# Kernel optimization log

Hardware: AMD Instinct MI355X
Metric: run time of the kernel (lower is better)

The kernel has to match this reference:

```python
import jax, jax.numpy as jnp
import numpy as np
from jax import lax

B, N, S, K, C, OUT = 8, 4096, 1024, 24, 64, 128
IN = 2 * C + 3  # 131: grouped(C+3) concat anchor feature(C)
EPS_BN = 1e-5


def _bn_params(key, c):
    k1, k2, k3, k4 = jax.random.split(key, 4)
    gamma = jax.random.uniform(k1, (c,), minval=0.5, maxval=1.5)
    beta = jax.random.normal(k2, (c,)) * 0.1
    mean = jax.random.normal(k3, (c,)) * 0.1
    var = jax.random.uniform(k4, (c,), minval=0.5, maxval=1.5)
    return jnp.stack([gamma, beta, mean, var])  # [4,c]


def setup_inputs() -> dict:
    key = jax.random.key(0)
    ks = jax.random.split(key, 20)
    w = lambda k, shp: jax.random.normal(k, shp) * 0.05
    inp = {
        "xyz": jax.random.normal(ks[0], (B, N, 3)),
        "points": jax.random.normal(ks[1], (B, N, C)),
        "affine_alpha": jnp.ones((1, 1, 1, C + 3)),
        "affine_beta": jnp.zeros((1, 1, 1, C + 3)),
        "transfer_w": w(ks[2], (OUT, IN)),
        "transfer_b": jnp.zeros((OUT,)),
        "transfer_bn": _bn_params(ks[3], OUT),
        "pre_w1": w(ks[4], (2, OUT, OUT)),
        "pre_b1": jnp.zeros((2, OUT)),
        "pre_bn1": jnp.stack([_bn_params(ks[5], OUT), _bn_params(ks[6], OUT)]),
        "pre_w2": w(ks[7], (2, OUT, OUT)),
        "pre_b2": jnp.zeros((2, OUT)),
        "pre_bn2": jnp.stack([_bn_params(ks[8], OUT), _bn_params(ks[9], OUT)]),
        "pos_w1": w(ks[10], (2, OUT, OUT)),
        "pos_b1": jnp.zeros((2, OUT)),
        "pos_bn1": jnp.stack([_bn_params(ks[11], OUT), _bn_params(ks[12], OUT)]),
        "pos_w2": w(ks[13], (2, OUT, OUT)),
        "pos_b2": jnp.zeros((2, OUT)),
        "pos_bn2": jnp.stack([_bn_params(ks[14], OUT), _bn_params(ks[15], OUT)]),
    }
    return inp


def _gather(x, idx):
    # x: [B,N,D], idx: [B,...] -> [B,...,D]
    return jax.vmap(lambda a, i: a[i])(x, idx)


def _sqdist(a, b):
    # a: [B,S,3], b: [B,N,3] -> [B,S,N]
    return (jnp.sum(a * a, -1)[:, :, None] + jnp.sum(b * b, -1)[:, None, :]
            - 2.0 * jnp.einsum('bsd,bnd->bsn', a, b))


def _fps(xyz, s):
    # furthest point sampling, starts at index 0 (matches CUDA pointnet2 impl)
    b, n, _ = xyz.shape
    def step(carry, _):
        dist, last = carry
        p = jnp.take_along_axis(xyz, last[:, None, None], axis=1)  # [B,1,3]
        d = jnp.sum((xyz - p) ** 2, -1)
        dist = jnp.minimum(dist, d)
        nxt = jnp.argmax(dist, axis=-1).astype(jnp.int32)
        return (dist, nxt), nxt
    init = (jnp.full((b, n), 1e10, xyz.dtype), jnp.zeros((b,), jnp.int32))
    _, idxs = lax.scan(step, init, None, length=s - 1)  # [S-1,B]
    return jnp.concatenate([jnp.zeros((1, b), jnp.int32), idxs], 0).T  # [B,S]


def _conv_bn(x, w, b, bn, act=True):
    # 1x1 Conv1d + BatchNorm (eval mode) + optional ReLU. x: [M,Cin,L]
    y = jnp.einsum('oc,mcl->mol', w, x) + b[None, :, None]
    g, be, mu, var = bn[0], bn[1], bn[2], bn[3]
    y = (y - mu[None, :, None]) * (g[None, :, None] / jnp.sqrt(var[None, :, None] + EPS_BN)) + be[None, :, None]
    return jax.nn.relu(y) if act else y


def _res_block(x, w1, b1, bn1, w2, b2, bn2):
    y = _conv_bn(x, w1, b1, bn1, act=True)
    y = _conv_bn(y, w2, b2, bn2, act=False)
    return jax.nn.relu(y + x)


def reference(xyz, points, affine_alpha, affine_beta,
              transfer_w, transfer_b, transfer_bn,
              pre_w1, pre_b1, pre_bn1, pre_w2, pre_b2, pre_bn2,
              pos_w1, pos_b1, pos_bn1, pos_w2, pos_b2, pos_bn2):
    b, n, _ = xyz.shape
    # ---- LocalGrouper ----
    fps_idx = _fps(xyz, S)                      # [B,S]
    new_xyz = _gather(xyz, fps_idx)             # [B,S,3]
    new_points = _gather(points, fps_idx)       # [B,S,C]
    d = _sqdist(new_xyz, xyz)                   # [B,S,N]
    _, idx = lax.top_k(-d, K)                   # k nearest -> [B,S,K]
    grouped_xyz = _gather(xyz, idx)             # [B,S,K,3]
    grouped_points = _gather(points, idx)       # [B,S,K,C]
    grouped = jnp.concatenate([grouped_points, grouped_xyz], -1)  # [B,S,K,C+3]
    # anchor normalize
    mean = jnp.concatenate([new_points, new_xyz], -1)[:, :, None, :]
    diff = grouped - mean
    std = jnp.std(diff.reshape(b, -1), axis=-1, ddof=1)[:, None, None, None]
    grouped = affine_alpha * (diff / (std + 1e-5)) + affine_beta
    anchor = jnp.broadcast_to(new_points[:, :, None, :], (b, S, K, C))
    feats = jnp.concatenate([grouped, anchor], -1)  # [B,S,K,2C+3]
    # ---- PreExtraction ----
    x = feats.transpose(0, 1, 3, 2).reshape(b * S, IN, K)  # [B*S,131,K]
    x = _conv_bn(x, transfer_w, transfer_b, transfer_bn, act=True)
    for i in range(2):
        x = _res_block(x, pre_w1[i], pre_b1[i], pre_bn1[i], pre_w2[i], pre_b2[i], pre_bn2[i])
    x = jnp.max(x, axis=-1)                     # adaptive max pool over K
    x = x.reshape(b, S, OUT).transpose(0, 2, 1)  # [B,OUT,S]
    # ---- PosExtraction ----
    for i in range(2):
        x = _res_block(x, pos_w1[i], pos_b1[i], pos_bn1[i], pos_w2[i], pos_b2[i], pos_bn2[i])
    return x  # [B,128,1024]
```

## Files before the change

### kernel.cpp

```cpp
#include <hip/hip_runtime.h>
#include <hip/hip_bf16.h>
#include <stdint.h>
#include <math.h>

#define DEVINL static __device__ __forceinline__

static constexpr int BB = 8, NN = 4096, SS = 1024, KK = 24, CC = 64;
static constexpr int INCH = 131, OUTCH = 128;

typedef __attribute__((ext_vector_type(8))) short short8v;
typedef __attribute__((ext_vector_type(4))) float f32x4;

#define MFMA16(a, b, c) __builtin_amdgcn_mfma_f32_16x16x32_bf16(a, b, c, 0, 0, 0)

DEVINL unsigned short f2bf(float v) {
  __hip_bfloat16 h = __float2bfloat16(v);
  return *reinterpret_cast<unsigned short*>(&h);
}
DEVINL float bfbits2f(unsigned short u) {
  unsigned x = ((unsigned)u) << 16;
  return __int_as_float(x);
}

__global__ __launch_bounds__(256) void k_prep_xyz(
    const float* __restrict__ xyz,
    float* __restrict__ xs, float* __restrict__ ys,
    float* __restrict__ zs, float* __restrict__ sb) {
  int e = blockIdx.x * 256 + threadIdx.x;
  if (e >= BB * NN) return;
  float x = xyz[e * 3 + 0];
  float y = xyz[e * 3 + 1];
  float z = xyz[e * 3 + 2];
  xs[e] = x; ys[e] = y; zs[e] = z;
  sb[e] = __fadd_rn(__fadd_rn(__fmul_rn(x, x), __fmul_rn(y, y)), __fmul_rn(z, z));
}

__global__ __launch_bounds__(256) void k_prep_w(
    const float* __restrict__ tw,
    const float* __restrict__ pw1, const float* __restrict__ pw2,
    const float* __restrict__ qw1, const float* __restrict__ qw2,
    const float* __restrict__ tb,  const float* __restrict__ tbn,
    const float* __restrict__ pb1, const float* __restrict__ pbn1,
    const float* __restrict__ pb2, const float* __restrict__ pbn2,
    const float* __restrict__ qb1, const float* __restrict__ qbn1,
    const float* __restrict__ qb2, const float* __restrict__ qbn2,
    float* __restrict__ wt_sq, float* __restrict__ bnsb,
    unsigned short* __restrict__ wfhi, unsigned short* __restrict__ wflo) {
  int e = blockIdx.x * 256 + threadIdx.x;
  const int NSQ = 8 * 128 * 128;
  const int NBN = 9 * 128;
  const int NFR = 168 * 64;
  if (e < NSQ) {
    int layer = e >> 14, m = e & 16383;
    int ci = m >> 7, co = m & 127;
    const float* src;
    switch (layer) {
      case 0: src = pw1;         break;
      case 1: src = pw2;         break;
      case 2: src = pw1 + 16384; break;
      case 3: src = pw2 + 16384; break;
      case 4: src = qw1;         break;
      case 5: src = qw2;         break;
      case 6: src = qw1 + 16384; break;
      default: src = qw2 + 16384; break;
    }
    wt_sq[layer * 16384 + ci * 128 + co] = src[co * 128 + ci];
  } else if (e < NSQ + NBN) {
    int r = e - NSQ;
    int L = r >> 7, co = r & 127;
    const float *bn, *bc;
    switch (L) {
      case 0: bn = tbn;        bc = tb;        break;
      case 1: bn = pbn1;       bc = pb1;       break;
      case 2: bn = pbn2;       bc = pb2;       break;
      case 3: bn = pbn1 + 512; bc = pb1 + 128; break;
      case 4: bn = pbn2 + 512; bc = pb2 + 128; break;
      case 5: bn = qbn1;       bc = qb1;       break;
      case 6: bn = qbn2;       bc = qb2;       break;
      case 7: bn = qbn1 + 512; bc = qb1 + 128; break;
      default: bn = qbn2 + 512; bc = qb2 + 128; break;
    }
    float g  = bn[co];
    float be = bn[128 + co];
    float mu = bn[256 + co];
    float va = bn[384 + co];
    float bcv = bc[co];
    float sc = g / sqrtf(va + 1e-5f);
    float bi = (bcv - mu) * sc + be;
    bnsb[L * 256 + co] = sc;
    bnsb[L * 256 + 128 + co] = bi;
  } else if (e < NSQ + NBN + NFR) {
    int r = e - (NSQ + NBN);
    int T = r >> 6, lane = r & 63;
    int L, ks, mt;
    if (T < 40) { L = 0; ks = T >> 3; mt = T & 7; }
    else { int r2 = T - 40; L = 1 + (r2 >> 5); int r3 = r2 & 31; ks = r3 >> 3; mt = r3 & 7; }
    const float* src;
    int K, stride;
    switch (L) {
      case 0:  src = tw;          K = 131; stride = 131; break;
      case 1:  src = pw1;         K = 128; stride = 128; break;
      case 2:  src = pw2;         K = 128; stride = 128; break;
      case 3:  src = pw1 + 16384; K = 128; stride = 128; break;
      default: src = pw2 + 16384; K = 128; stride = 128; break;
    }
    int m = lane & 15, kb = lane >> 4;
    int co = mt * 16 + m;
    int base = (T * 64 + lane) * 8;
#pragma unroll
    for (int j = 0; j < 8; j++) {
      int ci = ks * 32 + kb * 8 + j;
      float w = (ci < K) ? src[co * stride + ci] : 0.f;
      unsigned short h = f2bf(w);
      unsigned short l = f2bf(w - bfbits2f(h));
      wfhi[base + j] = h;
      wflo[base + j] = l;
    }
  }
}

DEVINL float wave_max_f32_l63(float x) {
#define STEPF(C)                                                                \
  {                                                                             \
    int o = __builtin_amdgcn_update_dpp(0xff800000, __float_as_int(x), C, 0xf, 0xf, false); \
    x = fmaxf(x, __int_as_float(o));                                            \
  }
  STEPF(0x111) STEPF(0x112) STEPF(0x114) STEPF(0x118) STEPF(0x142) STEPF(0x143)
#undef STEPF
  return x;
}

__global__ __launch_bounds__(256, 1) void k_fps(
    const float* __restrict__ xs, const float* __restrict__ ys,
    const float* __restrict__ zs, const float* __restrict__ sb,
    const float* __restrict__ points,
    float* __restrict__ nxyz, float* __restrict__ sa, float* __restrict__ newp) {
  __shared__ float lxl[NN], lyl[NN], lzl[NN];
  __shared__ unsigned long long pk[2][4];
  __shared__ int fpsl[SS];
  const int b = blockIdx.x, t = threadIdx.x;
  const int wid = t >> 6, lane = t & 63;
  const float* bx = xs + b * NN;
  const float* by = ys + b * NN;
  const float* bz = zs + b * NN;
  float rx[16], ry[16], rz[16], d[16];
  const int n0 = t * 16;
#pragma unroll
  for (int j = 0; j < 16; j++) {
    rx[j] = bx[n0 + j]; ry[j] = by[n0 + j]; rz[j] = bz[n0 + j];
    lxl[n0 + j] = rx[j]; lyl[n0 + j] = ry[j]; lzl[n0 + j] = rz[j];
    d[j] = 1e10f;
  }
  __syncthreads();
  float px = lxl[0], py = lyl[0], pz = lzl[0];
  if (t == 0) fpsl[0] = 0;
#pragma unroll 1
  for (int i = 1; i < SS; i++) {
    float bestval = -1.f;
    int bestn = 0;
#pragma unroll
    for (int j = 0; j < 16; j++) {
      float dx = __fsub_rn(rx[j], px);
      float dy = __fsub_rn(ry[j], py);
      float dz = __fsub_rn(rz[j], pz);
      float dd = __fadd_rn(__fadd_rn(__fmul_rn(dx, dx), __fmul_rn(dy, dy)),
                           __fmul_rn(dz, dz));
      float nd = fminf(d[j], dd);
      d[j] = nd;
      if (nd > bestval) { bestval = nd; bestn = n0 + j; }
    }
    float wmax = __int_as_float(
        __builtin_amdgcn_readlane(__float_as_int(wave_max_f32_l63(bestval)), 63));
    unsigned long long el = __ballot(bestval == wmax);
    int fl = (int)__ffsll(el) - 1;
    int wn = __builtin_amdgcn_readlane(bestn, fl);
    if (lane == 0)
      pk[i & 1][wid] = ((unsigned long long)__float_as_uint(wmax) << 32) |
                       (unsigned)(NN - 1 - wn);
    __syncthreads();
    const unsigned long long* P = pk[i & 1];
    unsigned long long k0 = P[0], k1 = P[1], k2 = P[2], k3 = P[3];
    unsigned long long m01 = k1 > k0 ? k1 : k0;
    unsigned long long m23 = k3 > k2 ? k3 : k2;
    unsigned long long g = m23 > m01 ? m23 : m01;
    int n = NN - 1 - (int)(unsigned)g;
    px = lxl[n]; py = lyl[n]; pz = lzl[n];
    if (t == 0) fpsl[i] = n;
  }
  __syncthreads();
  for (int s = t; s < SS; s += 256) {
    int row = fpsl[s];
    nxyz[(b * SS + s) * 3 + 0] = lxl[row];
    nxyz[(b * SS + s) * 3 + 1] = lyl[row];
    nxyz[(b * SS + s) * 3 + 2] = lzl[row];
    sa[b * SS + s] = sb[b * NN + row];
  }
  for (int e = t; e < SS * CC; e += 256) {
    int s = e >> 6, c = e & 63;
    int row = fpsl[s];
    newp[(b * SS + s) * CC + c] = points[(b * NN + row) * CC + c];
  }
}

__global__ __launch_bounds__(256, 2) void k_knn(
    const float* __restrict__ xs, const float* __restrict__ ys,
    const float* __restrict__ zs,
    const float* __restrict__ nxyz, const float* __restrict__ sa,
    const float* __restrict__ points, const float* __restrict__ newp,
    int* __restrict__ knn, double* __restrict__ spart) {
  __shared__ float lx[NN], ly[NN], lz[NN];
  __shared__ int selk[4][KK];
  const int blk = blockIdx.x, t = threadIdx.x, wid = t >> 6, lane = t & 63;
  const int b = blk >> 8;
  for (int e = t; e < NN; e += 256) {
    lx[e] = xs[b * NN + e]; ly[e] = ys[b * NN + e]; lz[e] = zs[b * NN + e];
  }
  __syncthreads();
  const int q = blk * 4 + wid;
  float qx = nxyz[q * 3 + 0], qy = nxyz[q * 3 + 1], qz = nxyz[q * 3 + 2];
  float qa = sa[q];
  unsigned keys[64];
#pragma unroll
  for (int j = 0; j < 64; j++) {
    int n = j * 64 + lane;
    float x = lx[n], y = ly[n], z = lz[n];
    float sbn = __fadd_rn(__fadd_rn(__fmul_rn(x, x), __fmul_rn(y, y)), __fmul_rn(z, z));
    float dot = __fadd_rn(__fadd_rn(__fmul_rn(qx, x), __fmul_rn(qy, y)), __fmul_rn(qz, z));
    float dd = __fsub_rn(__fadd_rn(qa, sbn), __fmul_rn(2.0f, dot));
    unsigned u = __float_as_uint(dd);
    u ^= (0x80000000u | (unsigned)((int)u >> 31));
    keys[j] = u;
  }
#pragma unroll 1
  for (int r = 0; r < KK; r++) {
    unsigned bv = keys[0];
    int bj = 0;
#pragma unroll
    for (int j = 1; j < 64; j++) {
      if (keys[j] < bv) { bv = keys[j]; bj = j; }
    }
    unsigned long long gk = ((unsigned long long)bv << 32) | (unsigned)(bj * 64 + lane);
#pragma unroll
    for (int m = 1; m < 64; m <<= 1) {
      unsigned long long o = __shfl_xor(gk, m);
      gk = o < gk ? o : gk;
    }
    int n = (int)(unsigned)gk;
    if (lane == 0) { knn[q * KK + r] = n; selk[wid][r] = n; }
    if (lane == (n & 63)) {
      int jj = n >> 6;
#pragma unroll
      for (int j = 0; j < 64; j++)
        if (j == jj) keys[j] = 0xFFFFFFFFu;
    }
  }
  double s1 = 0.0, s2 = 0.0;
#pragma unroll 1
  for (int i = 0; i < 26; i++) {
    int e = lane + 64 * i;
    if (e < KK * 67) {
      int k = e / 67, c = e - k * 67;
      int n = selk[wid][k];
      float g, mm;
      if (c < CC) {
        g = points[(b * NN + n) * CC + c];
        mm = newp[q * CC + c];
      } else {
        int cc = c - CC;
        g = cc == 0 ? lx[n] : (cc == 1 ? ly[n] : lz[n]);
        mm = nxyz[q * 3 + cc];
      }
      float v = __fsub_rn(g, mm);
      s1 += (double)v;
      s2 += (double)v * (double)v;
    }
  }
#pragma unroll
  for (int m = 1; m < 64; m <<= 1) {
    s1 += __shfl_xor(s1, m);
    s2 += __shfl_xor(s2, m);
  }
  if (lane == 0) { spart[q * 2 + 0] = s1; spart[q * 2 + 1] = s2; }
}

__global__ __launch_bounds__(256) void k_stdfin(
    const double* __restrict__ spart, float* __restrict__ stdp) {
  __shared__ double a1[256], a2[256];
  const int b = blockIdx.x, t = threadIdx.x;
  double s1 = 0.0, s2 = 0.0;
  for (int i = t; i < SS; i += 256) {
    s1 += spart[(b * SS + i) * 2 + 0];
    s2 += spart[(b * SS + i) * 2 + 1];
  }
  a1[t] = s1; a2[t] = s2;
  __syncthreads();
  for (int w = 128; w > 0; w >>= 1) {
    if (t < w) { a1[t] += a1[t + w]; a2[t] += a2[t + w]; }
    __syncthreads();
  }
  if (t == 0) {
    const double n = (double)SS * KK * 67;
    double m = a1[0] / n;
    double var = (a2[0] - a1[0] * m) / (n - 1.0);
    if (var < 0.0) var = 0.0;
    float stdf = (float)sqrt(var);
    stdp[b] = stdf + 1e-5f;
  }
}

static constexpr int BST = 168;
static constexpr int XST = 132;

__global__ __launch_bounds__(256, 3) void k_pre(
    const float* __restrict__ points,
    const float* __restrict__ alpha, const float* __restrict__ beta,
    const float* __restrict__ xs, const float* __restrict__ ys, const float* __restrict__ zs,
    const float* __restrict__ nxyz, const float* __restrict__ newp,
    const float* __restrict__ stdp, const int* __restrict__ knn,
    const unsigned short* __restrict__ wfhi, const unsigned short* __restrict__ wflo,
    const float* __restrict__ bnsb, float* __restrict__ pre_out) {
  __shared__ unsigned short Bhi[32 * BST];
  __shared__ unsigned short Blo[32 * BST];
  __shared__ float Xres[32 * XST];
  __shared__ int kn[KK];
  __shared__ float npl[CC], nxl[3], al[67], bt[67];
  __shared__ float stds;
  const int q = blockIdx.x, b = q >> 10, t = threadIdx.x;
  for (int e = t; e < 32 * BST; e += 256) { Bhi[e] = 0; Blo[e] = 0; }
  if (t < KK) kn[t] = knn[q * KK + t];
  if (t < 67) { al[t] = alpha[t]; bt[t] = beta[t]; }
  if (t < CC) npl[t] = newp[q * CC + t];
  if (t < 3) nxl[t] = nxyz[q * 3 + t];
  if (t == 0) stds = stdp[b];
  __syncthreads();
  for (int e = t; e < KK * 67; e += 256) {
    int k = e / 67, c = e - k * 67;
    int n = kn[k];
    float g, mm;
    if (c < CC) {
      g = points[(b * NN + n) * CC + c];
      mm = npl[c];
    } else {
      int cc = c - CC;
      g = cc == 0 ? xs[b * NN + n] : (cc == 1 ? ys[b * NN + n] : zs[b * NN + n]);
      mm = nxl[cc];
    }
    float v = __fsub_rn(g, mm);
    float tt = __fdiv_rn(v, stds);
    float val = __fadd_rn(__fmul_rn(al[c], tt), bt[c]);
    unsigned short h = f2bf(val);
    Bhi[k * BST + c] = h;
    Blo[k * BST + c] = f2bf(val - bfbits2f(h));
  }
  for (int e = t; e < CC * KK; e += 256) {
    int c = e / KK, k = e - c * KK;
    float val = npl[c];
    unsigned short h = f2bf(val);
    Bhi[k * BST + 67 + c] = h;
    Blo[k * BST + 67 + c] = f2bf(val - bfbits2f(h));
  }
  __syncthreads();

  const int wv = t >> 6, lane = t & 63;
  const int g4 = lane >> 4;
  const int l15 = lane & 15;
  const int mt0 = wv * 2;

#pragma unroll 1
  for (int L = 0; L < 5; ++L) {
    const int nks = (L == 0) ? 5 : 4;
    const int wtb = (L == 0) ? 0 : (8 + 32 * L);
    const bool addres = (L == 2) || (L == 4);
    const bool wres = (L == 0) || (L == 2);
    const bool pool = (L == 4);
    f32x4 acc00 = {0.f, 0.f, 0.f, 0.f}, acc01 = {0.f, 0.f, 0.f, 0.f};
    f32x4 acc10 = {0.f, 0.f, 0.f, 0.f}, acc11 = {0.f, 0.f, 0.f, 0.f};
#pragma unroll 1
    for (int ks = 0; ks < nks; ++ks) {
      const int tb = (wtb + ks * 8 + mt0) * 64 + lane;
      short8v wh0 = *(const short8v*)(wfhi + tb * 8);
      short8v wh1 = *(const short8v*)(wfhi + (tb + 64) * 8);
      short8v wl0 = *(const short8v*)(wflo + tb * 8);
      short8v wl1 = *(const short8v*)(wflo + (tb + 64) * 8);
      const int bo = l15 * BST + ks * 32 + g4 * 8;
      short8v bh0 = *(const short8v*)&Bhi[bo];
      short8v bh1 = *(const short8v*)&Bhi[bo + 16 * BST];
      short8v bl0 = *(const short8v*)&Blo[bo];
      short8v bl1 = *(const short8v*)&Blo[bo + 16 * BST];
      acc00 = MFMA16(wh0, bh0, acc00);
      acc00 = MFMA16(wl0, bh0, acc00);
      acc00 = MFMA16(wh0, bl0, acc00);
      acc01 = MFMA16(wh0, bh1, acc01);
      acc01 = MFMA16(wl0, bh1, acc01);
      acc01 = MFMA16(wh0, bl1, acc01);
      acc10 = MFMA16(wh1, bh0, acc10);
      acc10 = MFMA16(wl1, bh0, acc10);
      acc10 = MFMA16(wh1, bl0, acc10);
      acc11 = MFMA16(wh1, bh1, acc11);
      acc11 = MFMA16(wl1, bh1, acc11);
      acc11 = MFMA16(wh1, bl1, acc11);
    }
    __syncthreads();
    float mx0[4] = {0.f, 0.f, 0.f, 0.f};
    float mx1[4] = {0.f, 0.f, 0.f, 0.f};
    auto ep = [&](const f32x4& a, int mt_i, int nt, float* mxr) {
      const int co0 = (mt0 + mt_i) * 16 + g4 * 4;
      const int kp = nt * 16 + l15;
      const bool valid = kp < KK;
      f32x4 scv = *(const f32x4*)(bnsb + L * 256 + co0);
      f32x4 biv = *(const f32x4*)(bnsb + L * 256 + 128 + co0);
      float y[4];
#pragma unroll
      for (int r = 0; r < 4; r++) y[r] = fmaf(a[r], scv[r], biv[r]);
      if (addres && valid) {
        f32x4 xr = *(const f32x4*)&Xres[kp * XST + co0];
#pragma unroll
        for (int r = 0; r < 4; r++) y[r] += xr[r];
      }
#pragma unroll
      for (int r = 0; r < 4; r++) y[r] = fmaxf(y[r], 0.f);
      if (wres && valid) {
        f32x4 o = {y[0], y[1], y[2], y[3]};
        *(f32x4*)&Xres[kp * XST + co0] = o;
      }
      if (!pool) {
        if (valid) {
          unsigned h01 = (unsigned)f2bf(y[0]) | ((unsigned)f2bf(y[1]) << 16);
          unsigned h23 = (unsigned)f2bf(y[2]) | ((unsigned)f2bf(y[3]) << 16);
          *(uint2*)&Bhi[kp * BST + co0] = make_uint2(h01, h23);
          unsigned l01 = (unsigned)f2bf(y[0] - bfbits2f((unsigned short)(h01 & 0xffff))) |
                         ((unsigned)f2bf(y[1] - bfbits2f((unsigned short)(h01 >> 16))) << 16);
          unsigned l23 = (unsigned)f2bf(y[2] - bfbits2f((unsigned short)(h23 & 0xffff))) |
                         ((unsigned)f2bf(y[3] - bfbits2f((unsigned short)(h23 >> 16))) << 16);
          *(uint2*)&Blo[kp * BST + co0] = make_uint2(l01, l23);
        }
      } else {
#pragma unroll
        for (int r = 0; r < 4; r++) {
          float v = valid ? y[r] : 0.f;
          mxr[r] = fmaxf(mxr[r], v);
        }
      }
    };
    ep(acc00, 0, 0, mx0);
    ep(acc01, 0, 1, mx0);
    ep(acc10, 1, 0, mx1);
    ep(acc11, 1, 1, mx1);
    if (!pool) {
      __syncthreads();
    } else {
#pragma unroll
      for (int dstep = 1; dstep < 16; dstep <<= 1) {
#pragma unroll
        for (int r = 0; r < 4; r++) {
          mx0[r] = fmaxf(mx0[r], __shfl_xor(mx0[r], dstep));
          mx1[r] = fmaxf(mx1[r], __shfl_xor(mx1[r], dstep));
        }
      }
      if (l15 == 0) {
        f32x4 o0 = {mx0[0], mx0[1], mx0[2], mx0[3]};
        f32x4 o1 = {mx1[0], mx1[1], mx1[2], mx1[3]};
        *(f32x4*)&pre_out[q * 128 + mt0 * 16 + g4 * 4] = o0;
        *(f32x4*)&pre_out[q * 128 + (mt0 + 1) * 16 + g4 * 4] = o1;
      }
    }
  }
}

__global__ __launch_bounds__(256, 2) void k_pos(
    const float* __restrict__ pre_out, const float* __restrict__ wt_sq,
    const float* __restrict__ bnsb, float* __restrict__ out) {
  __shared__ float X[128][68];
  __shared__ float Y[128][68];
  const int blk = blockIdx.x, t = threadIdx.x;
  const int b = blk >> 4, s0 = (blk & 15) << 6;
  for (int e = t; e < 128 * 64; e += 256) {
    int sl = e >> 7, c = e & 127;
    X[c][sl] = pre_out[(b * SS + s0 + sl) * 128 + c];
  }
  __syncthreads();
  const int co0 = (t >> 3) << 2, p0 = (t & 7) << 3;
  float acc[4][8];
  auto conv = [&](const float (*IN)[68], const float* wt) {
#pragma unroll
    for (int i = 0; i < 4; i++)
#pragma unroll
      for (int j = 0; j < 8; j++) acc[i][j] = 0.f;
#pragma unroll 2
    for (int ci = 0; ci < 128; ci++) {
      float4 w = *(const float4*)(wt + ci * 128 + co0);
      float4 r0 = *(const float4*)&IN[ci][p0];
      float4 r1 = *(const float4*)&IN[ci][p0 + 4];
      float a[8] = {r0.x, r0.y, r0.z, r0.w, r1.x, r1.y, r1.z, r1.w};
#pragma unroll
      for (int j = 0; j < 8; j++) {
        acc[0][j] = fmaf(w.x, a[j], acc[0][j]);
        acc[1][j] = fmaf(w.y, a[j], acc[1][j]);
        acc[2][j] = fmaf(w.z, a[j], acc[2][j]);
        acc[3][j] = fmaf(w.w, a[j], acc[3][j]);
      }
    }
  };
  conv(X, wt_sq + 4 * 16384);
  {
    const float* bn = bnsb + 5 * 256;
#pragma unroll
    for (int i = 0; i < 4; i++) {
      float sc = bn[co0 + i], bi = bn[128 + co0 + i];
#pragma unroll
      for (int j = 0; j < 8; j++)
        Y[co0 + i][p0 + j] = fmaxf(fmaf(acc[i][j], sc, bi), 0.f);
    }
  }
  __syncthreads();
  conv(Y, wt_sq + 5 * 16384);
  {
    const float* bn = bnsb + 6 * 256;
#pragma unroll
    for (int i = 0; i < 4; i++) {
      float sc = bn[co0 + i], bi = bn[128 + co0 + i];
#pragma unroll
      for (int j = 0; j < 8; j++)
        X[co0 + i][p0 + j] =
            fmaxf(fmaf(acc[i][j], sc, bi) + X[co0 + i][p0 + j], 0.f);
    }
  }
  __syncthreads();
  conv(X, wt_sq + 6 * 16384);
  {
    const float* bn = bnsb + 7 * 256;
#pragma unroll
    for (int i = 0; i < 4; i++) {
      float sc = bn[co0 + i], bi = bn[128 + co0 + i];
#pragma unroll
      for (int j = 0; j < 8; j++)
        Y[co0 + i][p0 + j] = fmaxf(fmaf(acc[i][j], sc, bi), 0.f);
    }
  }
  __syncthreads();
  conv(Y, wt_sq + 7 * 16384);
  {
    const float* bn = bnsb + 8 * 256;
#pragma unroll
    for (int i = 0; i < 4; i++) {
      float sc = bn[co0 + i], bi = bn[128 + co0 + i];
      float4 o0, o1;
      float v;
      v = fmaxf(fmaf(acc[i][0], sc, bi) + X[co0 + i][p0 + 0], 0.f); o0.x = v;
      v = fmaxf(fmaf(acc[i][1], sc, bi) + X[co0 + i][p0 + 1], 0.f); o0.y = v;
      v = fmaxf(fmaf(acc[i][2], sc, bi) + X[co0 + i][p0 + 2], 0.f); o0.z = v;
      v = fmaxf(fmaf(acc[i][3], sc, bi) + X[co0 + i][p0 + 3], 0.f); o0.w = v;
      v = fmaxf(fmaf(acc[i][4], sc, bi) + X[co0 + i][p0 + 4], 0.f); o1.x = v;
      v = fmaxf(fmaf(acc[i][5], sc, bi) + X[co0 + i][p0 + 5], 0.f); o1.y = v;
      v = fmaxf(fmaf(acc[i][6], sc, bi) + X[co0 + i][p0 + 6], 0.f); o1.z = v;
      v = fmaxf(fmaf(acc[i][7], sc, bi) + X[co0 + i][p0 + 7], 0.f); o1.w = v;
      float* op = &out[(size_t)(b * 128 + co0 + i) * SS + s0 + p0];
      *(float4*)op = o0;
      *(float4*)(op + 4) = o1;
    }
  }
}

extern "C" void kernel_launch(void* const* d_in, const int* in_sizes, int n_in,
                              void* d_out, int out_size, void* d_ws, size_t ws_size,
                              hipStream_t stream) {
  (void)in_sizes; (void)n_in; (void)out_size; (void)ws_size;
  const float* xyz    = (const float*)d_in[0];
  const float* points = (const float*)d_in[1];
  const float* alpha  = (const float*)d_in[2];
  const float* beta   = (const float*)d_in[3];
  const float* tw     = (const float*)d_in[4];
  const float* tb     = (const float*)d_in[5];
  const float* tbn    = (const float*)d_in[6];
  const float* pw1    = (const float*)d_in[7];
  const float* pb1    = (const float*)d_in[8];
  const float* pbn1   = (const float*)d_in[9];
  const float* pw2    = (const float*)d_in[10];
  const float* pb2    = (const float*)d_in[11];
  const float* pbn2   = (const float*)d_in[12];
  const float* qw1    = (const float*)d_in[13];
  const float* qb1    = (const float*)d_in[14];
  const float* qbn1   = (const float*)d_in[15];
  const float* qw2    = (const float*)d_in[16];
  const float* qb2    = (const float*)d_in[17];
  const float* qbn2   = (const float*)d_in[18];

  char* ws = (char*)d_ws;
  size_t off = 0;
  auto alloc = [&](size_t bytes) -> char* {
    char* p = ws + off;
    off += (bytes + 255) & ~(size_t)255;
    return p;
  };
  float*  xs    = (float*)alloc(BB * NN * 4);
  float*  ys    = (float*)alloc(BB * NN * 4);
  float*  zs    = (float*)alloc(BB * NN * 4);
  float*  sb    = (float*)alloc(BB * NN * 4);
  float*  wt_sq = (float*)alloc(8 * 16384 * 4);
  float*  bnsb  = (float*)alloc(9 * 256 * 4);
  unsigned short* wfhi = (unsigned short*)alloc(168 * 512 * 2);
  unsigned short* wflo = (unsigned short*)alloc(168 * 512 * 2);
  float*  nxyz  = (float*)alloc(BB * SS * 3 * 4);
  float*  sa    = (float*)alloc(BB * SS * 4);
  float*  newp  = (float*)alloc(BB * SS * CC * 4);
  int*    knn   = (int*)alloc(BB * SS * KK * 4);
  double* spart = (double*)alloc(BB * SS * 2 * 8);
  float*  stdp  = (float*)alloc(256);
  float*  preo  = (float*)alloc((size_t)BB * SS * 128 * 4);
  float*  out   = (float*)d_out;

  const int prep_n = 8 * 128 * 128 + 9 * 128 + 168 * 64;
  hipLaunchKernelGGL(k_prep_xyz, dim3((BB * NN + 255) / 256), dim3(256), 0, stream,
                     xyz, xs, ys, zs, sb);
  hipLaunchKernelGGL(k_prep_w, dim3((prep_n + 255) / 256), dim3(256), 0, stream,
                     tw, pw1, pw2, qw1, qw2, tb, tbn, pb1, pbn1, pb2, pbn2,
                     qb1, qbn1, qb2, qbn2, wt_sq, bnsb, wfhi, wflo);
  hipLaunchKernelGGL(k_fps, dim3(BB), dim3(256), 0, stream,
                     xs, ys, zs, sb, points, nxyz, sa, newp);
  hipLaunchKernelGGL(k_knn, dim3(BB * SS / 4), dim3(256), 0, stream,
                     xs, ys, zs, nxyz, sa, points, newp, knn, spart);
  hipLaunchKernelGGL(k_stdfin, dim3(BB), dim3(256), 0, stream, spart, stdp);
  hipLaunchKernelGGL(k_pre, dim3(BB * SS), dim3(256), 0, stream,
                     points, alpha, beta, xs, ys, zs, nxyz, newp, stdp, knn,
                     wfhi, wflo, bnsb, preo);
  hipLaunchKernelGGL(k_pos, dim3(BB * SS / 64), dim3(256), 0, stream,
                     preo, wt_sq, bnsb, out);
}
```

Before: 1.063 ms.

## Truncate bf16 hi/lo split, tree-reduce FPS argmax, unroll layer loop

Replaces round-to-nearest bf16 conversion in the hi/lo split with bit truncation, so the split needs only masks and shifts. Rewrites the per-thread FPS argmax as a pairwise tree reduction instead of a serial compare chain, shortening the dependency path in the sequential sampling loop. Fully unrolls the five-layer MLP loop so per-layer constants become compile-time values. The tree reduction's tie-breaking still prefers the lower index, and the truncated split still represents the value with a hi+lo pair. Full unrolling increases code size and register pressure.

```diff
diff --git a/kernel.cpp b/kernel.cpp
--- a/kernel.cpp
+++ b/kernel.cpp
@@ -13,13 +13,15 @@
 
 #define MFMA16(a, b, c) __builtin_amdgcn_mfma_f32_16x16x32_bf16(a, b, c, 0, 0, 0)
 
-DEVINL unsigned short f2bf(float v) {
-  __hip_bfloat16 h = __float2bfloat16(v);
-  return *reinterpret_cast<unsigned short*>(&h);
-}
-DEVINL float bfbits2f(unsigned short u) {
-  unsigned x = ((unsigned)u) << 16;
-  return __int_as_float(x);
+DEVINL unsigned short bfhi(float v) {
+  return (unsigned short)(__float_as_uint(v) >> 16);
+}
+DEVINL float bfhif(float v) {
+  return __uint_as_float(__float_as_uint(v) & 0xFFFF0000u);
+}
+DEVINL unsigned short bflo(float v) {
+  float r = __fsub_rn(v, bfhif(v));
+  return (unsigned short)(__float_as_uint(r) >> 16);
 }
 
 __global__ __launch_bounds__(256) void k_prep_xyz(
@@ -111,10 +113,8 @@
     for (int j = 0; j < 8; j++) {
       int ci = ks * 32 + kb * 8 + j;
       float w = (ci < K) ? src[co * stride + ci] : 0.f;
-      unsigned short h = f2bf(w);
-      unsigned short l = f2bf(w - bfbits2f(h));
-      wfhi[base + j] = h;
-      wflo[base + j] = l;
+      wfhi[base + j] = bfhi(w);
+      wflo[base + j] = bflo(w);
     }
   }
 }
@@ -156,8 +156,6 @@
   if (t == 0) fpsl[0] = 0;
 #pragma unroll 1
   for (int i = 1; i < SS; i++) {
-    float bestval = -1.f;
-    int bestn = 0;
 #pragma unroll
     for (int j = 0; j < 16; j++) {
       float dx = __fsub_rn(rx[j], px);
@@ -165,10 +163,32 @@
       float dz = __fsub_rn(rz[j], pz);
       float dd = __fadd_rn(__fadd_rn(__fmul_rn(dx, dx), __fmul_rn(dy, dy)),
                            __fmul_rn(dz, dz));
-      float nd = fminf(d[j], dd);
-      d[j] = nd;
-      if (nd > bestval) { bestval = nd; bestn = n0 + j; }
-    }
+      d[j] = fminf(d[j], dd);
+    }
+    float v8[8]; int i8[8];
+#pragma unroll
+    for (int j = 0; j < 8; j++) {
+      bool c = d[2 * j] >= d[2 * j + 1];
+      v8[j] = c ? d[2 * j] : d[2 * j + 1];
+      i8[j] = c ? (2 * j) : (2 * j + 1);
+    }
+    float v4[4]; int i4[4];
+#pragma unroll
+    for (int j = 0; j < 4; j++) {
+      bool c = v8[2 * j] >= v8[2 * j + 1];
+      v4[j] = c ? v8[2 * j] : v8[2 * j + 1];
+      i4[j] = c ? i8[2 * j] : i8[2 * j + 1];
+    }
+    float v2[2]; int i2[2];
+#pragma unroll
+    for (int j = 0; j < 2; j++) {
+      bool c = v4[2 * j] >= v4[2 * j + 1];
+      v2[j] = c ? v4[2 * j] : v4[2 * j + 1];
+      i2[j] = c ? i4[2 * j] : i4[2 * j + 1];
+    }
+    bool c0 = v2[0] >= v2[1];
+    float bestval = c0 ? v2[0] : v2[1];
+    int bestn = n0 + (c0 ? i2[0] : i2[1]);
     float wmax = __int_as_float(
         __builtin_amdgcn_readlane(__float_as_int(wave_max_f32_l63(bestval)), 63));
     unsigned long long el = __ballot(bestval == wmax);
@@ -348,16 +368,14 @@
     float v = __fsub_rn(g, mm);
     float tt = __fdiv_rn(v, stds);
     float val = __fadd_rn(__fmul_rn(al[c], tt), bt[c]);
-    unsigned short h = f2bf(val);
-    Bhi[k * BST + c] = h;
-    Blo[k * BST + c] = f2bf(val - bfbits2f(h));
+    Bhi[k * BST + c] = bfhi(val);
+    Blo[k * BST + c] = bflo(val);
   }
   for (int e = t; e < CC * KK; e += 256) {
     int c = e / KK, k = e - c * KK;
     float val = npl[c];
-    unsigned short h = f2bf(val);
-    Bhi[k * BST + 67 + c] = h;
-    Blo[k * BST + 67 + c] = f2bf(val - bfbits2f(h));
+    Bhi[k * BST + 67 + c] = bfhi(val);
+    Blo[k * BST + 67 + c] = bflo(val);
   }
   __syncthreads();
 
@@ -366,7 +384,7 @@
   const int l15 = lane & 15;
   const int mt0 = wv * 2;
 
-#pragma unroll 1
+#pragma unroll
   for (int L = 0; L < 5; ++L) {
     const int nks = (L == 0) ? 5 : 4;
     const int wtb = (L == 0) ? 0 : (8 + 32 * L);
@@ -425,13 +443,17 @@
       }
       if (!pool) {
         if (valid) {
-          unsigned h01 = (unsigned)f2bf(y[0]) | ((unsigned)f2bf(y[1]) << 16);
-          unsigned h23 = (unsigned)f2bf(y[2]) | ((unsigned)f2bf(y[3]) << 16);
+          unsigned b0 = __float_as_uint(y[0]), b1 = __float_as_uint(y[1]);
+          unsigned b2 = __float_as_uint(y[2]), b3 = __float_as_uint(y[3]);
+          unsigned h01 = (b0 >> 16) | (b1 & 0xFFFF0000u);
+          unsigned h23 = (b2 >> 16) | (b3 & 0xFFFF0000u);
           *(uint2*)&Bhi[kp * BST + co0] = make_uint2(h01, h23);
-          unsigned l01 = (unsigned)f2bf(y[0] - bfbits2f((unsigned short)(h01 & 0xffff))) |
-                         ((unsigned)f2bf(y[1] - bfbits2f((unsigned short)(h01 >> 16))) << 16);
-          unsigned l23 = (unsigned)f2bf(y[2] - bfbits2f((unsigned short)(h23 & 0xffff))) |
-                         ((unsigned)f2bf(y[3] - bfbits2f((unsigned short)(h23 >> 16))) << 16);
+          float r0 = __fsub_rn(y[0], __uint_as_float(b0 & 0xFFFF0000u));
+          float r1 = __fsub_rn(y[1], __uint_as_float(b1 & 0xFFFF0000u));
+          float r2 = __fsub_rn(y[2], __uint_as_float(b2 & 0xFFFF0000u));
+          float r3 = __fsub_rn(y[3], __uint_as_float(b3 & 0xFFFF0000u));
+          unsigned l01 = (__float_as_uint(r0) >> 16) | (__float_as_uint(r1) & 0xFFFF0000u);
+          unsigned l23 = (__float_as_uint(r2) >> 16) | (__float_as_uint(r3) & 0xFFFF0000u);
           *(uint2*)&Blo[kp * BST + co0] = make_uint2(l01, l23);
         }
       } else {
```

New measurement: 1.208 ms. 1.14x slower.
